# Optimization experiments

Measured on AMD Instinct MI355X. Metric: run time of the kernel, lower is better.

## Reference

```python
import jax, jax.numpy as jnp
import numpy as np

B, S, D, E, K = 2, 2048, 1024, 8, 2
H = 4 * D  # FFN hidden


def setup_inputs() -> dict:
    key = jax.random.key(0)
    ks = jax.random.split(key, 6)
    x = jax.random.normal(ks[0], (B, S, D), dtype=jnp.float32)
    # xavier-uniform gate
    lim_g = np.sqrt(6.0 / (D + E)).astype(np.float32)
    W_gate = jax.random.uniform(ks[1], (D, E), minval=-lim_g, maxval=lim_g, dtype=jnp.float32)
    # per-expert FFN params, stacked on leading expert axis
    lim1 = np.sqrt(1.0 / D).astype(np.float32)
    lim2 = np.sqrt(1.0 / H).astype(np.float32)
    W1 = jax.random.uniform(ks[2], (E, D, H), minval=-lim1, maxval=lim1, dtype=jnp.float32)
    b1 = jax.random.uniform(ks[3], (E, H), minval=-lim1, maxval=lim1, dtype=jnp.float32)
    W2 = jax.random.uniform(ks[4], (E, H, D), minval=-lim2, maxval=lim2, dtype=jnp.float32)
    b2 = jax.random.uniform(ks[5], (E, D), minval=-lim2, maxval=lim2, dtype=jnp.float32)
    return {"x": x, "W_gate": W_gate, "W1": W1, "b1": b1, "W2": W2, "b2": b2}


def reference(x, W_gate, W1, b1, W2, b2):
    # gating: topk mask then softmax over kept logits
    gate = jnp.einsum('bsd,de->bse', x, W_gate)                      # [B,S,E]
    kth = jax.lax.top_k(gate, K)[0][..., -1:]                        # k-th largest [B,S,1]
    mask = jax.nn.softmax(jnp.where(gate >= kth, gate, -jnp.inf), axis=-1)
    # all-experts FFN (faithful to original dense compute)
    h = jax.nn.relu(jnp.einsum('bsd,edh->bseh', x, W1) + b1)         # [B,S,E,H]
    y = jnp.einsum('bseh,ehd->bsed', h, W2) + b2                     # [B,S,E,D]
    # masked MEAN over experts (original uses .mean, i.e. divides by E)
    return (y * mask[..., None]).mean(axis=-2)                       # [B,S,D]
```

## Files before the change

kernel.cpp:

```cpp
#include <hip/hip_runtime.h>
#include <stdint.h>
#include <stddef.h>

#define TOK   4096
#define DDIM  1024
#define EXP   8
#define HDIM  4096

typedef __bf16 bf16x8 __attribute__((ext_vector_type(8)));
typedef __bf16 bf16x4 __attribute__((ext_vector_type(4)));
typedef float  f32x4  __attribute__((ext_vector_type(4)));

#define OFF_COUNTS 0ull
#define OFF_PREFIX 256ull
#define OFF_PERM   512ull
#define OFF_WGT    (OFF_PERM + 131072ull)
#define OFF_XBF    (OFF_WGT + 131072ull)
#define OFF_W1T    (OFF_XBF + 8388608ull)
#define OFF_W2T    (OFF_W1T + 67108864ull)
#define OFF_HBF    (OFF_W2T + 67108864ull)
#define OFF_T2E    (OFF_HBF + 68157440ull)

__device__ __forceinline__ void load16_lds(const void* g, void* l) {
  __builtin_amdgcn_global_load_lds((__attribute__((address_space(1))) void*)g,
                                   (__attribute__((address_space(3))) void*)l,
                                   16, 0, 0);
}

__global__ __launch_bounds__(256) void gate_kernel(
    const float* __restrict__ x, const float* __restrict__ Wg,
    __bf16* __restrict__ x_bf, int* __restrict__ counts,
    int* __restrict__ perm, float* __restrict__ wgt,
    int4* __restrict__ tok2exp)
{
  const int lane = threadIdx.x & 63;
  const int wid  = threadIdx.x >> 6;
  const int t    = blockIdx.x * 4 + wid;
  const float* xr = x + (size_t)t * DDIM;

  float acc[EXP];
#pragma unroll
  for (int e = 0; e < EXP; ++e) acc[e] = 0.f;

#pragma unroll
  for (int it = 0; it < 4; ++it) {
    const int d0 = it * 256 + lane * 4;
    float4 xv = *(const float4*)(xr + d0);
    bf16x4 xb = { (__bf16)xv.x, (__bf16)xv.y, (__bf16)xv.z, (__bf16)xv.w };
    *(bf16x4*)(x_bf + (size_t)t * DDIM + d0) = xb;
    const float* wrow = Wg + (size_t)d0 * EXP;
    float xs[4] = { xv.x, xv.y, xv.z, xv.w };
#pragma unroll
    for (int u = 0; u < 4; ++u) {
      float4 wa = *(const float4*)(wrow + u * 8);
      float4 wb = *(const float4*)(wrow + u * 8 + 4);
      acc[0] += xs[u] * wa.x; acc[1] += xs[u] * wa.y;
      acc[2] += xs[u] * wa.z; acc[3] += xs[u] * wa.w;
      acc[4] += xs[u] * wb.x; acc[5] += xs[u] * wb.y;
      acc[6] += xs[u] * wb.z; acc[7] += xs[u] * wb.w;
    }
  }
#pragma unroll
  for (int e = 0; e < EXP; ++e) {
    float v = acc[e];
#pragma unroll
    for (int s = 32; s > 0; s >>= 1) v += __shfl_down(v, s, 64);
    acc[e] = v;
  }
  if (lane == 0) {
    int e0 = 0; float g0 = acc[0];
#pragma unroll
    for (int e = 1; e < EXP; ++e) if (acc[e] > g0) { g0 = acc[e]; e0 = e; }
    int e1 = 0; float g1 = -3.4e38f;
#pragma unroll
    for (int e = 0; e < EXP; ++e) if (e != e0 && acc[e] > g1) { g1 = acc[e]; e1 = e; }
    float ex = __expf(g1 - g0);
    float m0 = 1.f / (1.f + ex);
    float m1 = ex  / (1.f + ex);
    int p0 = atomicAdd(&counts[e0], 1);
    perm[e0 * TOK + p0] = t;  wgt[e0 * TOK + p0] = m0 * 0.125f;
    int p1 = atomicAdd(&counts[e1], 1);
    perm[e1 * TOK + p1] = t;  wgt[e1 * TOK + p1] = m1 * 0.125f;
    tok2exp[t] = make_int4(e0, p0, e1, p1);
  }
}

__global__ void prefix_kernel(const int* __restrict__ counts, int* __restrict__ prefix)
{
  if (threadIdx.x == 0 && blockIdx.x == 0) {
    int s = 0;
    for (int e = 0; e < EXP; ++e) { prefix[e] = s; s += counts[e]; }
    prefix[EXP] = s;
  }
}

__global__ __launch_bounds__(256) void transpose2_kernel(
    const float* __restrict__ W1, const float* __restrict__ W2,
    __bf16* __restrict__ W1t, __bf16* __restrict__ W2t)
{
  __shared__ float tile[64 * 65];
  const int bid   = blockIdx.x;
  const int which = bid >> 13;
  const int e     = (bid >> 10) & 7;
  const int t10   = bid & 1023;
  const float* src; __bf16* dst; int Kd, Nd, tk, tn;
  if (which == 0) { Kd = 1024; Nd = 4096; src = W1; dst = W1t; tk = t10 & 15; tn = t10 >> 4; }
  else            { Kd = 4096; Nd = 1024; src = W2; dst = W2t; tk = t10 >> 4; tn = t10 & 15; }
  const int k0 = tk * 64, n0 = tn * 64;
  src += ((size_t)e * Kd + k0) * Nd + n0;
  dst += ((size_t)e * Nd + n0) * Kd + k0;

  const int tid = threadIdx.x;
  const int lr = tid >> 4, lc = (tid & 15) * 4;
#pragma unroll
  for (int p = 0; p < 4; ++p) {
    const int r = p * 16 + lr;
    float4 v = *(const float4*)(src + (size_t)r * Nd + lc);
    tile[r * 65 + lc + 0] = v.x;
    tile[r * 65 + lc + 1] = v.y;
    tile[r * 65 + lc + 2] = v.z;
    tile[r * 65 + lc + 3] = v.w;
  }
  __syncthreads();
  const int n = tid >> 2, kcb = (tid & 3) * 8;
#pragma unroll
  for (int h = 0; h < 2; ++h) {
    const int kb = kcb + h * 32;
    bf16x8 o;
#pragma unroll
    for (int u = 0; u < 8; ++u) o[u] = (__bf16)tile[(kb + u) * 65 + n];
    *(bf16x8*)(dst + (size_t)n * Kd + kb) = o;
  }
}

__global__ __launch_bounds__(256, 2) void gemm1_kernel(
    const __bf16* __restrict__ x_bf, const __bf16* __restrict__ W1t,
    const float* __restrict__ b1, __bf16* __restrict__ h_bf,
    const int* __restrict__ perm, const int* __restrict__ counts,
    const int* __restrict__ prefix)
{
  const int bid = blockIdx.x;
  const int e   = bid >> 10;
  const int mt  = (bid >> 5) & 31;
  const int nt  = bid & 31;
  const int cnt = counts[e];
  if (mt * 128 >= cnt) return;
  const int pfx = prefix[e];

  __shared__ __align__(16) __bf16 As[4096];
  __shared__ __align__(16) __bf16 Bs[4096];

  const int tid  = threadIdx.x;
  const int lane = tid & 63, wid = tid >> 6;
  const int wm = wid & 1, wn = wid >> 1;
  const int qd = lane >> 4, l15 = lane & 15;

  const int rA0 = tid >> 2, rA1 = rA0 + 64;
  const int pA0 = (tid & 3) ^ ((rA0 >> 1) & 3);
  const int pA1 = (tid & 3) ^ ((rA1 >> 1) & 3);
  int mA0 = mt * 128 + rA0; if (mA0 >= cnt) mA0 = cnt - 1;
  int mA1 = mt * 128 + rA1; if (mA1 >= cnt) mA1 = cnt - 1;
  const int tok0 = perm[e * TOK + mA0];
  const int tok1 = perm[e * TOK + mA1];
  const __bf16* gA0 = x_bf + (size_t)tok0 * DDIM + pA0 * 8;
  const __bf16* gA1 = x_bf + (size_t)tok1 * DDIM + pA1 * 8;
  const __bf16* Wte = W1t + (size_t)e * HDIM * DDIM;
  const __bf16* gB0 = Wte + (size_t)(nt * 128 + rA0) * DDIM + pA0 * 8;
  const __bf16* gB1 = Wte + (size_t)(nt * 128 + rA1) * DDIM + pA1 * 8;
  __bf16* ldsA0 = &As[tid * 8];
  __bf16* ldsA1 = &As[(tid + 256) * 8];
  __bf16* ldsB0 = &Bs[tid * 8];
  __bf16* ldsB1 = &Bs[(tid + 256) * 8];

  f32x4 acc[4][4] = {};

  for (int kk = 0; kk < DDIM; kk += 32) {
    __syncthreads();
    load16_lds(gA0 + kk, ldsA0);
    load16_lds(gA1 + kk, ldsA1);
    load16_lds(gB0 + kk, ldsB0);
    load16_lds(gB1 + kk, ldsB1);
    __syncthreads();
    bf16x8 af[4], bfr[4];
#pragma unroll
    for (int i = 0; i < 4; ++i) {
      int r = wm * 64 + i * 16 + l15;
      int ch = r * 4 + (qd ^ ((r >> 1) & 3));
      af[i] = *(const bf16x8*)(As + ch * 8);
    }
#pragma unroll
    for (int j = 0; j < 4; ++j) {
      int r = wn * 64 + j * 16 + l15;
      int ch = r * 4 + (qd ^ ((r >> 1) & 3));
      bfr[j] = *(const bf16x8*)(Bs + ch * 8);
    }
#pragma unroll
    for (int i = 0; i < 4; ++i)
#pragma unroll
      for (int j = 0; j < 4; ++j)
        acc[i][j] = __builtin_amdgcn_mfma_f32_16x16x32_bf16(af[i], bfr[j], acc[i][j], 0, 0, 0);
  }

  const float* b1e = b1 + (size_t)e * HDIM;
#pragma unroll
  for (int i = 0; i < 4; ++i) {
#pragma unroll
    for (int v = 0; v < 4; ++v) {
      const int rl = wm * 64 + i * 16 + qd * 4 + v;
      const int m  = mt * 128 + rl;
      if (m < cnt) {
        __bf16* hrow = h_bf + (size_t)(pfx + m) * HDIM;
#pragma unroll
        for (int j = 0; j < 4; ++j) {
          const int col = nt * 128 + wn * 64 + j * 16 + l15;
          float hv = acc[i][j][v] + b1e[col];
          hv = fmaxf(hv, 0.f);
          hrow[col] = (__bf16)hv;
        }
      }
    }
  }
}

__global__ __launch_bounds__(256, 2) void gemm2_kernel(
    const __bf16* __restrict__ h_bf, const __bf16* __restrict__ W2t,
    float* __restrict__ Y,
    const int* __restrict__ counts, const int* __restrict__ prefix)
{
  const int bid = blockIdx.x;
  const int ks  = bid & 1;
  const int nt  = (bid >> 1) & 7;
  const int mt  = (bid >> 4) & 31;
  const int e   = bid >> 9;
  const int cnt = counts[e];
  if (mt * 128 >= cnt) return;
  const int pfx = prefix[e];

  __shared__ __align__(16) __bf16 As[4096];
  __shared__ __align__(16) __bf16 Bs[4096];

  const int tid  = threadIdx.x;
  const int lane = tid & 63, wid = tid >> 6;
  const int wm = wid & 1, wn = wid >> 1;
  const int qd = lane >> 4, l15 = lane & 15;

  const int rA0 = tid >> 2, rA1 = rA0 + 64;
  const int pA0 = (tid & 3) ^ ((rA0 >> 1) & 3);
  const int pA1 = (tid & 3) ^ ((rA1 >> 1) & 3);
  const __bf16* gA0 = h_bf + (size_t)(pfx + mt * 128 + rA0) * HDIM + pA0 * 8;
  const __bf16* gA1 = h_bf + (size_t)(pfx + mt * 128 + rA1) * HDIM + pA1 * 8;
  const __bf16* Wte = W2t + (size_t)e * DDIM * HDIM;
  const __bf16* gB0 = Wte + (size_t)(nt * 128 + rA0) * HDIM + pA0 * 8;
  const __bf16* gB1 = Wte + (size_t)(nt * 128 + rA1) * HDIM + pA1 * 8;
  __bf16* ldsA0 = &As[tid * 8];
  __bf16* ldsA1 = &As[(tid + 256) * 8];
  __bf16* ldsB0 = &Bs[tid * 8];
  __bf16* ldsB1 = &Bs[(tid + 256) * 8];

  f32x4 acc[4][4] = {};

  const int kbeg = ks * (HDIM / 2);
  const int kend = kbeg + (HDIM / 2);
  for (int kk = kbeg; kk < kend; kk += 32) {
    __syncthreads();
    load16_lds(gA0 + kk, ldsA0);
    load16_lds(gA1 + kk, ldsA1);
    load16_lds(gB0 + kk, ldsB0);
    load16_lds(gB1 + kk, ldsB1);
    __syncthreads();
    bf16x8 af[4], bfr[4];
#pragma unroll
    for (int i = 0; i < 4; ++i) {
      int r = wm * 64 + i * 16 + l15;
      int ch = r * 4 + (qd ^ ((r >> 1) & 3));
      af[i] = *(const bf16x8*)(As + ch * 8);
    }
#pragma unroll
    for (int j = 0; j < 4; ++j) {
      int r = wn * 64 + j * 16 + l15;
      int ch = r * 4 + (qd ^ ((r >> 1) & 3));
      bfr[j] = *(const bf16x8*)(Bs + ch * 8);
    }
#pragma unroll
    for (int i = 0; i < 4; ++i)
#pragma unroll
      for (int j = 0; j < 4; ++j)
        acc[i][j] = __builtin_amdgcn_mfma_f32_16x16x32_bf16(af[i], bfr[j], acc[i][j], 0, 0, 0);
  }

  float* Ys = Y + (size_t)ks * (2 * TOK) * DDIM;
#pragma unroll
  for (int i = 0; i < 4; ++i) {
#pragma unroll
    for (int v = 0; v < 4; ++v) {
      const int rl = wm * 64 + i * 16 + qd * 4 + v;
      const int m  = mt * 128 + rl;
      if (m < cnt) {
        float* yrow = Ys + (size_t)(pfx + m) * DDIM;
#pragma unroll
        for (int j = 0; j < 4; ++j) {
          const int col = nt * 128 + wn * 64 + j * 16 + l15;
          yrow[col] = acc[i][j][v];
        }
      }
    }
  }
}

__global__ __launch_bounds__(256) void combine_kernel(
    const float* __restrict__ Y, const float* __restrict__ b2,
    const float* __restrict__ wgt, const int4* __restrict__ tok2exp,
    const int* __restrict__ prefix, float* __restrict__ out)
{
  const int t = blockIdx.x;
  const int c = threadIdx.x * 4;
  const int4 m = tok2exp[t];
  const int g0 = prefix[m.x] + m.y;
  const int g1 = prefix[m.z] + m.w;
  const float w0 = wgt[m.x * TOK + m.y];
  const float w1 = wgt[m.z * TOK + m.w];
  const float* Y0 = Y;
  const float* Y1 = Y + (size_t)(2 * TOK) * DDIM;

  float4 a0 = *(const float4*)(Y0 + (size_t)g0 * DDIM + c);
  float4 a1 = *(const float4*)(Y1 + (size_t)g0 * DDIM + c);
  float4 c0 = *(const float4*)(Y0 + (size_t)g1 * DDIM + c);
  float4 c1 = *(const float4*)(Y1 + (size_t)g1 * DDIM + c);
  float4 be0 = *(const float4*)(b2 + (size_t)m.x * DDIM + c);
  float4 be1 = *(const float4*)(b2 + (size_t)m.z * DDIM + c);
  float4 r;
  r.x = w0 * (a0.x + a1.x + be0.x) + w1 * (c0.x + c1.x + be1.x);
  r.y = w0 * (a0.y + a1.y + be0.y) + w1 * (c0.y + c1.y + be1.y);
  r.z = w0 * (a0.z + a1.z + be0.z) + w1 * (c0.z + c1.z + be1.z);
  r.w = w0 * (a0.w + a1.w + be0.w) + w1 * (c0.w + c1.w + be1.w);
  *(float4*)(out + (size_t)t * DDIM + c) = r;
}

extern "C" void kernel_launch(void* const* d_in, const int* in_sizes, int n_in,
                              void* d_out, int out_size, void* d_ws, size_t ws_size,
                              hipStream_t stream)
{
  const float* x  = (const float*)d_in[0];
  const float* Wg = (const float*)d_in[1];
  const float* W1 = (const float*)d_in[2];
  const float* b1 = (const float*)d_in[3];
  const float* W2 = (const float*)d_in[4];
  const float* b2 = (const float*)d_in[5];
  float* out = (float*)d_out;

  char* ws = (char*)d_ws;
  int*    counts  = (int*)(ws + OFF_COUNTS);
  int*    prefix  = (int*)(ws + OFF_PREFIX);
  int*    perm    = (int*)(ws + OFF_PERM);
  float*  wgt     = (float*)(ws + OFF_WGT);
  __bf16* x_bf    = (__bf16*)(ws + OFF_XBF);
  __bf16* W1t     = (__bf16*)(ws + OFF_W1T);
  __bf16* W2t     = (__bf16*)(ws + OFF_W2T);
  __bf16* h_bf    = (__bf16*)(ws + OFF_HBF);
  int4*   tok2exp = (int4*)(ws + OFF_T2E);
  float*  Y       = (float*)(ws + OFF_W1T);

  hipMemsetAsync(counts, 0, 256, stream);

  gate_kernel<<<TOK / 4, 256, 0, stream>>>(x, Wg, x_bf, counts, perm, wgt, tok2exp);
  prefix_kernel<<<1, 64, 0, stream>>>(counts, prefix);
  transpose2_kernel<<<16384, 256, 0, stream>>>(W1, W2, W1t, W2t);
  gemm1_kernel<<<EXP * 32 * 32, 256, 0, stream>>>(x_bf, W1t, b1, h_bf, perm, counts, prefix);
  gemm2_kernel<<<EXP * 32 * 8 * 2, 256, 0, stream>>>(h_bf, W2t, Y, counts, prefix);
  combine_kernel<<<TOK, 256, 0, stream>>>(Y, b2, wgt, tok2exp, prefix, out);
}
```

Before: 647.5 us.

## Merge transpose into gate kernel, reorder GEMM grids, 4-way split-K with bf16 partials

Folds the weight transpose and gating into a single prep launch, removing one kernel launch. The GEMM block-index decode is reordered so consecutive blocks share an N tile, which improves weight reuse in L2. gemm2 moves from 2-way to 4-way split-K for more parallelism and writes its partials as bf16 instead of fp32, so combine now sums four bf16 slabs. The bf16 partials lose precision, and the Y workspace, which aliases the W1t region, has to fit four slabs.

Result: slower. 1.022 ms (+57.9%).

```diff
diff --git a/kernel.cpp b/kernel.cpp
--- a/kernel.cpp
+++ b/kernel.cpp
@@ -27,15 +27,55 @@
                                    16, 0, 0);
 }
 
-__global__ __launch_bounds__(256) void gate_kernel(
+__global__ __launch_bounds__(256) void prep_kernel(
+    const float* __restrict__ W1, const float* __restrict__ W2,
+    __bf16* __restrict__ W1t, __bf16* __restrict__ W2t,
     const float* __restrict__ x, const float* __restrict__ Wg,
     __bf16* __restrict__ x_bf, int* __restrict__ counts,
     int* __restrict__ perm, float* __restrict__ wgt,
     int4* __restrict__ tok2exp)
 {
-  const int lane = threadIdx.x & 63;
-  const int wid  = threadIdx.x >> 6;
-  const int t    = blockIdx.x * 4 + wid;
+  __shared__ float tile[64 * 65];
+  const int bid = blockIdx.x;
+  const int tid = threadIdx.x;
+
+  if (bid < 16384) {
+    const int which = bid >> 13;
+    const int e     = (bid >> 10) & 7;
+    const int t10   = bid & 1023;
+    const float* src; __bf16* dst; int Kd, Nd, tk, tn;
+    if (which == 0) { Kd = 1024; Nd = 4096; src = W1; dst = W1t; tk = t10 & 15; tn = t10 >> 4; }
+    else            { Kd = 4096; Nd = 1024; src = W2; dst = W2t; tk = t10 >> 4; tn = t10 & 15; }
+    const int k0 = tk * 64, n0 = tn * 64;
+    src += ((size_t)e * Kd + k0) * Nd + n0;
+    dst += ((size_t)e * Nd + n0) * Kd + k0;
+
+    const int lr = tid >> 4, lc = (tid & 15) * 4;
+#pragma unroll
+    for (int p = 0; p < 4; ++p) {
+      const int r = p * 16 + lr;
+      float4 v = *(const float4*)(src + (size_t)r * Nd + lc);
+      tile[r * 65 + lc + 0] = v.x;
+      tile[r * 65 + lc + 1] = v.y;
+      tile[r * 65 + lc + 2] = v.z;
+      tile[r * 65 + lc + 3] = v.w;
+    }
+    __syncthreads();
+    const int n = tid >> 2, kcb = (tid & 3) * 8;
+#pragma unroll
+    for (int h = 0; h < 2; ++h) {
+      const int kb = kcb + h * 32;
+      bf16x8 o;
+#pragma unroll
+      for (int u = 0; u < 8; ++u) o[u] = (__bf16)tile[(kb + u) * 65 + n];
+      *(bf16x8*)(dst + (size_t)n * Kd + kb) = o;
+    }
+    return;
+  }
+
+  const int lane = tid & 63;
+  const int wid  = tid >> 6;
+  const int t    = (bid - 16384) * 4 + wid;
   const float* xr = x + (size_t)t * DDIM;
 
   float acc[EXP];
@@ -94,45 +134,6 @@
   }
 }
 
-__global__ __launch_bounds__(256) void transpose2_kernel(
-    const float* __restrict__ W1, const float* __restrict__ W2,
-    __bf16* __restrict__ W1t, __bf16* __restrict__ W2t)
-{
-  __shared__ float tile[64 * 65];
-  const int bid   = blockIdx.x;
-  const int which = bid >> 13;
-  const int e     = (bid >> 10) & 7;
-  const int t10   = bid & 1023;
-  const float* src; __bf16* dst; int Kd, Nd, tk, tn;
-  if (which == 0) { Kd = 1024; Nd = 4096; src = W1; dst = W1t; tk = t10 & 15; tn = t10 >> 4; }
-  else            { Kd = 4096; Nd = 1024; src = W2; dst = W2t; tk = t10 >> 4; tn = t10 & 15; }
-  const int k0 = tk * 64, n0 = tn * 64;
-  src += ((size_t)e * Kd + k0) * Nd + n0;
-  dst += ((size_t)e * Nd + n0) * Kd + k0;
-
-  const int tid = threadIdx.x;
-  const int lr = tid >> 4, lc = (tid & 15) * 4;
-#pragma unroll
-  for (int p = 0; p < 4; ++p) {
-    const int r = p * 16 + lr;
-    float4 v = *(const float4*)(src + (size_t)r * Nd + lc);
-    tile[r * 65 + lc + 0] = v.x;
-    tile[r * 65 + lc + 1] = v.y;
-    tile[r * 65 + lc + 2] = v.z;
-    tile[r * 65 + lc + 3] = v.w;
-  }
-  __syncthreads();
-  const int n = tid >> 2, kcb = (tid & 3) * 8;
-#pragma unroll
-  for (int h = 0; h < 2; ++h) {
-    const int kb = kcb + h * 32;
-    bf16x8 o;
-#pragma unroll
-    for (int u = 0; u < 8; ++u) o[u] = (__bf16)tile[(kb + u) * 65 + n];
-    *(bf16x8*)(dst + (size_t)n * Kd + kb) = o;
-  }
-}
-
 __global__ __launch_bounds__(256, 2) void gemm1_kernel(
     const __bf16* __restrict__ x_bf, const __bf16* __restrict__ W1t,
     const float* __restrict__ b1, __bf16* __restrict__ h_bf,
@@ -141,8 +142,8 @@
 {
   const int bid = blockIdx.x;
   const int e   = bid >> 10;
-  const int mt  = (bid >> 5) & 31;
-  const int nt  = bid & 31;
+  const int nt  = (bid >> 5) & 31;
+  const int mt  = bid & 31;
   const int cnt = counts[e];
   if (mt * 128 >= cnt) return;
   const int pfx = prefix[e];
@@ -224,14 +225,14 @@
 
 __global__ __launch_bounds__(256, 2) void gemm2_kernel(
     const __bf16* __restrict__ h_bf, const __bf16* __restrict__ W2t,
-    float* __restrict__ Y,
+    __bf16* __restrict__ Y,
     const int* __restrict__ counts, const int* __restrict__ prefix)
 {
   const int bid = blockIdx.x;
-  const int ks  = bid & 1;
-  const int nt  = (bid >> 1) & 7;
-  const int mt  = (bid >> 4) & 31;
-  const int e   = bid >> 9;
+  const int mt  = bid & 31;
+  const int ks  = (bid >> 5) & 3;
+  const int nt  = (bid >> 7) & 7;
+  const int e   = bid >> 10;
   const int cnt = counts[e];
   if (mt * 128 >= cnt) return;
   const int pfx = prefix[e];
@@ -259,8 +260,8 @@
 
   f32x4 acc[4][4] = {};
 
-  const int kbeg = ks * (HDIM / 2);
-  const int kend = kbeg + (HDIM / 2);
+  const int kbeg = ks * (HDIM / 4);
+  const int kend = kbeg + (HDIM / 4);
   for (int kk = kbeg; kk < kend; kk += 32) {
     __syncthreads();
     load16_lds(gA0 + kk, ldsA0);
@@ -288,7 +289,7 @@
         acc[i][j] = __builtin_amdgcn_mfma_f32_16x16x32_bf16(af[i], bfr[j], acc[i][j], 0, 0, 0);
   }
 
-  float* Ys = Y + (size_t)ks * (2 * TOK) * DDIM;
+  __bf16* Ys = Y + (size_t)ks * (2 * TOK) * DDIM;
 #pragma unroll
   for (int i = 0; i < 4; ++i) {
 #pragma unroll
@@ -296,11 +297,11 @@
       const int rl = wm * 64 + i * 16 + qd * 4 + v;
       const int m  = mt * 128 + rl;
       if (m < cnt) {
-        float* yrow = Ys + (size_t)(pfx + m) * DDIM;
+        __bf16* yrow = Ys + (size_t)(pfx + m) * DDIM;
 #pragma unroll
         for (int j = 0; j < 4; ++j) {
           const int col = nt * 128 + wn * 64 + j * 16 + l15;
-          yrow[col] = acc[i][j][v];
+          yrow[col] = (__bf16)acc[i][j][v];
         }
       }
     }
@@ -308,7 +309,7 @@
 }
 
 __global__ __launch_bounds__(256) void combine_kernel(
-    const float* __restrict__ Y, const float* __restrict__ b2,
+    const __bf16* __restrict__ Y, const float* __restrict__ b2,
     const float* __restrict__ wgt, const int4* __restrict__ tok2exp,
     const int* __restrict__ prefix, float* __restrict__ out)
 {
@@ -319,20 +320,24 @@
   const int g1 = prefix[m.z] + m.w;
   const float w0 = wgt[m.x * TOK + m.y];
   const float w1 = wgt[m.z * TOK + m.w];
-  const float* Y0 = Y;
-  const float* Y1 = Y + (size_t)(2 * TOK) * DDIM;
-
-  float4 a0 = *(const float4*)(Y0 + (size_t)g0 * DDIM + c);
-  float4 a1 = *(const float4*)(Y1 + (size_t)g0 * DDIM + c);
-  float4 c0 = *(const float4*)(Y0 + (size_t)g1 * DDIM + c);
-  float4 c1 = *(const float4*)(Y1 + (size_t)g1 * DDIM + c);
+  const size_t slab = (size_t)(2 * TOK) * DDIM;
+
+  float s0x = 0.f, s0y = 0.f, s0z = 0.f, s0w = 0.f;
+  float s1x = 0.f, s1y = 0.f, s1z = 0.f, s1w = 0.f;
+#pragma unroll
+  for (int s = 0; s < 4; ++s) {
+    bf16x4 a = *(const bf16x4*)(Y + s * slab + (size_t)g0 * DDIM + c);
+    bf16x4 b = *(const bf16x4*)(Y + s * slab + (size_t)g1 * DDIM + c);
+    s0x += (float)a[0]; s0y += (float)a[1]; s0z += (float)a[2]; s0w += (float)a[3];
+    s1x += (float)b[0]; s1y += (float)b[1]; s1z += (float)b[2]; s1w += (float)b[3];
+  }
   float4 be0 = *(const float4*)(b2 + (size_t)m.x * DDIM + c);
   float4 be1 = *(const float4*)(b2 + (size_t)m.z * DDIM + c);
   float4 r;
-  r.x = w0 * (a0.x + a1.x + be0.x) + w1 * (c0.x + c1.x + be1.x);
-  r.y = w0 * (a0.y + a1.y + be0.y) + w1 * (c0.y + c1.y + be1.y);
-  r.z = w0 * (a0.z + a1.z + be0.z) + w1 * (c0.z + c1.z + be1.z);
-  r.w = w0 * (a0.w + a1.w + be0.w) + w1 * (c0.w + c1.w + be1.w);
+  r.x = w0 * (s0x + be0.x) + w1 * (s1x + be1.x);
+  r.y = w0 * (s0y + be0.y) + w1 * (s1y + be1.y);
+  r.z = w0 * (s0z + be0.z) + w1 * (s1z + be1.z);
+  r.w = w0 * (s0w + be0.w) + w1 * (s1w + be1.w);
   *(float4*)(out + (size_t)t * DDIM + c) = r;
 }
 
@@ -358,14 +363,14 @@
   __bf16* W2t     = (__bf16*)(ws + OFF_W2T);
   __bf16* h_bf    = (__bf16*)(ws + OFF_HBF);
   int4*   tok2exp = (int4*)(ws + OFF_T2E);
-  float*  Y       = (float*)(ws + OFF_W1T);
+  __bf16* Y       = (__bf16*)(ws + OFF_W1T);
 
   hipMemsetAsync(counts, 0, 256, stream);
 
-  gate_kernel<<<TOK / 4, 256, 0, stream>>>(x, Wg, x_bf, counts, perm, wgt, tok2exp);
+  prep_kernel<<<16384 + TOK / 4, 256, 0, stream>>>(W1, W2, W1t, W2t,
+                                                   x, Wg, x_bf, counts, perm, wgt, tok2exp);
   prefix_kernel<<<1, 64, 0, stream>>>(counts, prefix);
-  transpose2_kernel<<<16384, 256, 0, stream>>>(W1, W2, W1t, W2t);
   gemm1_kernel<<<EXP * 32 * 32, 256, 0, stream>>>(x_bf, W1t, b1, h_bf, perm, counts, prefix);
-  gemm2_kernel<<<EXP * 32 * 8 * 2, 256, 0, stream>>>(h_bf, W2t, Y, counts, prefix);
+  gemm2_kernel<<<EXP * 8 * 4 * 32, 256, 0, stream>>>(h_bf, W2t, Y, counts, prefix);
   combine_kernel<<<TOK, 256, 0, stream>>>(Y, b2, wgt, tok2exp, prefix, out);
 }
```
